# Optimization experiments

Measured on AMD Instinct MI355X. Metric: run time of the kernel, lower is better.

Reference implementation:

```python
import jax, jax.numpy as jnp
import numpy as np

N_ENT = 100000   # n_entities
N_REL = 40       # n_relations_ckg
D = 64           # embed_dim
L = 3            # n_layers
E = 1000000      # number of CKG triples (edges)


def setup_inputs() -> dict:
    key = jax.random.key(0)
    k = jax.random.split(key, 6)
    xavier = np.sqrt(6.0 / (D + D))  # xavier_uniform for square Linear
    return {
        "heads": jax.random.randint(k[0], (E,), 0, N_ENT),
        "rels": jax.random.randint(k[1], (E,), 0, N_REL),
        "tails": jax.random.randint(k[2], (E,), 0, N_ENT),
        "entity_embed": 0.01 * jax.random.normal(k[3], (N_ENT, D), dtype=jnp.float32),
        "rel_embeds": 0.01 * jax.random.normal(k[4], (L, N_REL, D), dtype=jnp.float32),
        "Ws": (jax.random.uniform(k[5], (L, D, D), minval=-1.0, maxval=1.0) * xavier).astype(jnp.float32),
    }


def _kgat_layer(h, heads, rels, tails, rel_emb, W):
    # h: [N, D]; heads/rels/tails: [E]; rel_emb: [n_rel, D]; W: [D, D] (nn.Linear weight)
    n = h.shape[0]
    e_h = h[heads]            # [E, D] gather
    e_t = h[tails]            # [E, D] gather
    e_r = rel_emb[rels]       # [E, D] gather
    # pi(h,r,t) = e_t . tanh(e_h + e_r)
    score = jnp.sum(e_t * jnp.tanh(e_h + e_r), axis=-1)          # [E]
    score = score - jax.lax.stop_gradient(jnp.max(score))        # global shift (detach)
    score_exp = jnp.exp(score)                                   # [E]
    score_sum = jax.ops.segment_sum(score_exp, heads, num_segments=n)  # [N]
    attn = score_exp / (score_sum[heads] + 1e-10)                # [E] per-head softmax
    agg = jax.ops.segment_sum(attn[:, None] * e_t, heads, num_segments=n)  # [N, D]
    out = (h + agg) @ W.T                                        # Linear, no bias
    return jax.nn.leaky_relu(out, negative_slope=0.2)            # dropout = identity (eval)


def reference(heads, rels, tails, entity_embed, rel_embeds, Ws):
    h = entity_embed
    all_layers = [h]
    for l in range(rel_embeds.shape[0]):
        h = _kgat_layer(h, heads, rels, tails, rel_embeds[l], Ws[l])
        all_layers.append(h)
    return jnp.concatenate(all_layers, axis=-1)  # [N, D*(L+1)]
```

## Files before the change

kernel.cpp:

```cpp
#include <hip/hip_runtime.h>

#define DD 64
#define ROW 256
#define CAP 32
#define CAPSH 5

__global__ void k_build(const float* __restrict__ ent, float* __restrict__ out,
                        const int* __restrict__ heads, const int* __restrict__ rels,
                        const int* __restrict__ tails, int* __restrict__ counts,
                        int* __restrict__ ovf, int* __restrict__ permpos,
                        int* __restrict__ packedF, int n_rows, int nE) {
    int idx = blockIdx.x * blockDim.x + threadIdx.x;
    int total = n_rows * 16;
    if (idx < total) {
        int n = idx >> 4, q = idx & 15;
        const float4* src = (const float4*)(ent + (long)n * DD);
        float4* dst = (float4*)(out + (long)n * ROW);
        dst[q] = src[q];
    }
    if (idx < nE) {
        int h = heads[idx];
        int rank = atomicAdd(counts + h, 1);
        permpos[idx] = rank;
        if (rank < CAP) packedF[((long)h << CAPSH) + rank] = tails[idx] | (rels[idx] << 20);
        else *ovf = 1;
    }
}

__global__ __launch_bounds__(1024) void k_fallback(
        const int* __restrict__ heads, const int* __restrict__ rels,
        const int* __restrict__ tails, const int* __restrict__ counts,
        const int* __restrict__ ovf, int* __restrict__ offs,
        const int* __restrict__ permpos, int* __restrict__ packed,
        int n, int nE) {
    if (*ovf == 0) return;
    __shared__ int lds[1024];
    int t = threadIdx.x;
    int per = (n + 1023) / 1024;
    int lo = t * per, hi = min(lo + per, n);
    int sum = 0;
    for (int i = lo; i < hi; ++i) sum += counts[i];
    lds[t] = sum; __syncthreads();
    for (int d = 1; d < 1024; d <<= 1) {
        int u = (t >= d) ? lds[t - d] : 0;
        __syncthreads();
        lds[t] += u;
        __syncthreads();
    }
    int run = lds[t] - sum;
    for (int i = lo; i < hi; ++i) { offs[i] = run; run += counts[i]; }
    if (t == 0) offs[n] = nE;
    __syncthreads();
    for (int e = t; e < nE; e += 1024) {
        int h = heads[e];
        packed[offs[h] + permpos[e]] = tails[e] | (rels[e] << 20);
    }
}

__global__ __launch_bounds__(256) void k_layer(
        const int* __restrict__ offs, const int* __restrict__ counts,
        const int* __restrict__ ovf, const int* __restrict__ packed,
        const float* __restrict__ hbase, const float* __restrict__ relemb,
        const float* __restrict__ W, float* __restrict__ outbase,
        int n_heads, int nE) {
    __shared__ float Wt[DD * 65];
    __shared__ float xs[4][DD];
    const int mode = *ovf;
    for (int idx = threadIdx.x; idx < DD * DD; idx += 256)
        Wt[(idx & 63) * 65 + (idx >> 6)] = W[idx];
    __syncthreads();

    const int cap = (n_heads << CAPSH) - 1;

    int w = threadIdx.x >> 6, lane = threadIdx.x & 63;
    int g = lane >> 4, s = lane & 15;

    for (int hd = blockIdx.x * 4 + w; hd < n_heads; hd += gridDim.x * 4) {
        int p0 = (mode == 0) ? (hd << CAPSH) : offs[hd];
        int vAll = packed[min(p0 + lane, cap)];
        int pe = (mode == 0) ? p0 + counts[hd] : offs[hd + 1];
        const float4 eh4 = *(const float4*)(hbase + (long)hd * ROW + 4 * s);
        float4 acc = make_float4(0.f, 0.f, 0.f, 0.f);
        float ssum = 0.f;

        for (int cbase = p0; cbase < pe; cbase += 64) {
            int clen = min(pe - cbase, 64);

            int i0 = (g < clen) ? g : 0;
            int i1 = (4 + g < clen) ? 4 + g : 0;
            int v0 = __shfl(vAll, i0);
            int v1 = __shfl(vAll, i1);
            float4 tt0 = *(const float4*)(hbase + (long)(v0 & 0xFFFFF) * ROW + 4 * s);
            float4 rr0 = *(const float4*)(relemb + (v0 >> 20) * DD + 4 * s);
            float4 tt1 = *(const float4*)(hbase + (long)(v1 & 0xFFFFF) * ROW + 4 * s);
            float4 rr1 = *(const float4*)(relemb + (v1 >> 20) * DD + 4 * s);

            for (int i = 0; i < clen; i += 8) {
                int ia = i + 8 + g;  ia = (ia < clen) ? ia : 0;
                int ib = i + 12 + g; ib = (ib < clen) ? ib : 0;
                int va = __shfl(vAll, ia);
                int vb = __shfl(vAll, ib);
                float4 tta = *(const float4*)(hbase + (long)(va & 0xFFFFF) * ROW + 4 * s);
                float4 rra = *(const float4*)(relemb + (va >> 20) * DD + 4 * s);
                float4 ttb = *(const float4*)(hbase + (long)(vb & 0xFFFFF) * ROW + 4 * s);
                float4 rrb = *(const float4*)(relemb + (vb >> 20) * DD + 4 * s);

                {
                    float sc = 0.f;
                    #pragma unroll
                    for (int q = 0; q < 4; ++q) {
                        float xq = (&eh4.x)[q] + (&rr0.x)[q];
                        float t = __expf(2.f * xq);
                        float th = 1.f - 2.f * __builtin_amdgcn_rcpf(t + 1.f);
                        sc += (&tt0.x)[q] * th;
                    }
                    #pragma unroll
                    for (int off = 1; off <= 8; off <<= 1) sc += __shfl_xor(sc, off);
                    float se = ((i + g) < clen) ? __expf(sc) : 0.f;
                    ssum += se;
                    acc.x += se * tt0.x; acc.y += se * tt0.y;
                    acc.z += se * tt0.z; acc.w += se * tt0.w;
                }
                {
                    float sc = 0.f;
                    #pragma unroll
                    for (int q = 0; q < 4; ++q) {
                        float xq = (&eh4.x)[q] + (&rr1.x)[q];
                        float t = __expf(2.f * xq);
                        float th = 1.f - 2.f * __builtin_amdgcn_rcpf(t + 1.f);
                        sc += (&tt1.x)[q] * th;
                    }
                    #pragma unroll
                    for (int off = 1; off <= 8; off <<= 1) sc += __shfl_xor(sc, off);
                    float se = ((i + 4 + g) < clen) ? __expf(sc) : 0.f;
                    ssum += se;
                    acc.x += se * tt1.x; acc.y += se * tt1.y;
                    acc.z += se * tt1.z; acc.w += se * tt1.w;
                }
                tt0 = tta; rr0 = rra; tt1 = ttb; rr1 = rrb;
            }

            if (cbase + 64 < pe) vAll = packed[min(cbase + 64 + lane, cap)];
        }

        #pragma unroll
        for (int off = 16; off <= 32; off <<= 1) {
            acc.x += __shfl_xor(acc.x, off);
            acc.y += __shfl_xor(acc.y, off);
            acc.z += __shfl_xor(acc.z, off);
            acc.w += __shfl_xor(acc.w, off);
            ssum  += __shfl_xor(ssum,  off);
        }
        float inv = 1.f / (ssum + 1e-10f);
        float4 x4;
        x4.x = eh4.x + acc.x * inv;  x4.y = eh4.y + acc.y * inv;
        x4.z = eh4.z + acc.z * inv;  x4.w = eh4.w + acc.w * inv;
        if (g == 0) *(float4*)(&xs[w][4 * s]) = x4;

        float y = 0.f;
        const float* xw = xs[w];
        #pragma unroll
        for (int k4 = 0; k4 < DD; k4 += 4) {
            float4 xv = *(const float4*)(xw + k4);
            y += xv.x * Wt[(k4 + 0) * 65 + lane];
            y += xv.y * Wt[(k4 + 1) * 65 + lane];
            y += xv.z * Wt[(k4 + 2) * 65 + lane];
            y += xv.w * Wt[(k4 + 3) * 65 + lane];
        }
        y = y >= 0.f ? y : 0.2f * y;
        outbase[(long)hd * ROW + lane] = y;
    }
}

extern "C" void kernel_launch(void* const* d_in, const int* in_sizes, int n_in,
                              void* d_out, int out_size, void* d_ws, size_t ws_size,
                              hipStream_t stream) {
    const int*   heads = (const int*)d_in[0];
    const int*   rels  = (const int*)d_in[1];
    const int*   tails = (const int*)d_in[2];
    const float* ent   = (const float*)d_in[3];
    const float* rel   = (const float*)d_in[4];
    const float* Ws    = (const float*)d_in[5];
    float* out = (float*)d_out;

    const int nE = in_sizes[0];
    const int N  = in_sizes[3] / DD;
    const int L  = in_sizes[5] / (DD * DD);
    const int NREL = in_sizes[4] / (L * DD);

    int* counts  = (int*)d_ws;
    int* ovf     = counts + N;
    int* offs    = ovf + 1;
    int* permpos = offs + (N + 1);
    int* packedF = permpos + nE;

    dim3 blk(256);
    int fuse_total = max(N * 16, nE);

    hipMemsetAsync(counts, 0, (size_t)(N + 1) * sizeof(int), stream);
    k_build<<<(fuse_total + 255) / 256, blk, 0, stream>>>(
        ent, out, heads, rels, tails, counts, ovf, permpos, packedF, N, nE);
    k_fallback<<<1, 1024, 0, stream>>>(
        heads, rels, tails, counts, ovf, offs, permpos, packedF, N, nE);

    for (int l = 0; l < L; ++l) {
        k_layer<<<2048, blk, 0, stream>>>(
            offs, counts, ovf, packedF, out + l * DD, rel + (long)l * NREL * DD,
            Ws + (long)l * DD * DD, out + (l + 1) * DD, N, nE);
    }
}
```

Before: 445.2 us.

## Use odd polynomial tanh when inputs are small, fuse entity copy into first layer

Computes the per-layer max |rel_emb| and, per head, the max |e_h|. When their sum stays below a bound, tanh is evaluated with an odd polynomial instead of exp plus reciprocal, with a plain loop kept as the fallback. The first layer now reads the entity table directly with a 64-float stride and writes the layer-0 slice of the output itself, so the separate copy pass disappears. The permpos array is dropped and the overflow path uses atomic cursors instead. The polynomial's accuracy depends on the range bound, which holds for small-magnitude embeddings like the test data.

```diff
diff --git a/kernel.cpp b/kernel.cpp
--- a/kernel.cpp
+++ b/kernel.cpp
@@ -4,35 +4,38 @@
 #define ROW 256
 #define CAP 32
 #define CAPSH 5
-
-__global__ void k_build(const float* __restrict__ ent, float* __restrict__ out,
-                        const int* __restrict__ heads, const int* __restrict__ rels,
+#define POLY_R 0.625f
+
+__global__ __launch_bounds__(256) void k_relmax(const float* __restrict__ rel,
+                                                float* __restrict__ maxrel, int per) {
+    __shared__ float red[256];
+    int t = threadIdx.x, l = blockIdx.x;
+    float m = 0.f;
+    for (int i = t; i < per; i += 256) m = fmaxf(m, __builtin_fabsf(rel[(long)l * per + i]));
+    red[t] = m; __syncthreads();
+    for (int d = 128; d > 0; d >>= 1) {
+        if (t < d) red[t] = fmaxf(red[t], red[t + d]);
+        __syncthreads();
+    }
+    if (t == 0) maxrel[l] = red[0];
+}
+
+__global__ void k_build(const int* __restrict__ heads, const int* __restrict__ rels,
                         const int* __restrict__ tails, int* __restrict__ counts,
-                        int* __restrict__ ovf, int* __restrict__ permpos,
-                        int* __restrict__ packedF, int n_rows, int nE) {
-    int idx = blockIdx.x * blockDim.x + threadIdx.x;
-    int total = n_rows * 16;
-    if (idx < total) {
-        int n = idx >> 4, q = idx & 15;
-        const float4* src = (const float4*)(ent + (long)n * DD);
-        float4* dst = (float4*)(out + (long)n * ROW);
-        dst[q] = src[q];
-    }
-    if (idx < nE) {
-        int h = heads[idx];
-        int rank = atomicAdd(counts + h, 1);
-        permpos[idx] = rank;
-        if (rank < CAP) packedF[((long)h << CAPSH) + rank] = tails[idx] | (rels[idx] << 20);
-        else *ovf = 1;
-    }
+                        int* __restrict__ ovf, int* __restrict__ packedF, int nE) {
+    int e = blockIdx.x * 256 + threadIdx.x;
+    if (e >= nE) return;
+    int h = heads[e];
+    int rank = atomicAdd(counts + h, 1);
+    if (rank < CAP) packedF[((long)h << CAPSH) + rank] = tails[e] | (rels[e] << 20);
+    else *ovf = 1;
 }
 
 __global__ __launch_bounds__(1024) void k_fallback(
         const int* __restrict__ heads, const int* __restrict__ rels,
         const int* __restrict__ tails, const int* __restrict__ counts,
         const int* __restrict__ ovf, int* __restrict__ offs,
-        const int* __restrict__ permpos, int* __restrict__ packed,
-        int n, int nE) {
+        int* __restrict__ cursors, int* __restrict__ packed, int n, int nE) {
     if (*ovf == 0) return;
     __shared__ int lds[1024];
     int t = threadIdx.x;
@@ -48,28 +51,34 @@
         __syncthreads();
     }
     int run = lds[t] - sum;
-    for (int i = lo; i < hi; ++i) { offs[i] = run; run += counts[i]; }
+    for (int i = lo; i < hi; ++i) { offs[i] = run; cursors[i] = run; run += counts[i]; }
     if (t == 0) offs[n] = nE;
     __syncthreads();
     for (int e = t; e < nE; e += 1024) {
-        int h = heads[e];
-        packed[offs[h] + permpos[e]] = tails[e] | (rels[e] << 20);
+        int pos = atomicAdd(cursors + heads[e], 1);
+        packed[pos] = tails[e] | (rels[e] << 20);
     }
 }
 
 __global__ __launch_bounds__(256) void k_layer(
         const int* __restrict__ offs, const int* __restrict__ counts,
         const int* __restrict__ ovf, const int* __restrict__ packed,
-        const float* __restrict__ hbase, const float* __restrict__ relemb,
+        const float* __restrict__ src, int srcsh, float* __restrict__ copy0,
+        const float* __restrict__ maxrel, const float* __restrict__ relemb,
         const float* __restrict__ W, float* __restrict__ outbase,
-        int n_heads, int nE) {
+        int n_heads) {
     __shared__ float Wt[DD * 65];
     __shared__ float xs[4][DD];
     const int mode = *ovf;
+    const float mr = *maxrel;
     for (int idx = threadIdx.x; idx < DD * DD; idx += 256)
         Wt[(idx & 63) * 65 + (idx >> 6)] = W[idx];
     __syncthreads();
 
+    const float c11 = -5.70498872745e-3f, c9 = 2.06390887954e-2f,
+                c7  = -5.37397155531e-2f, c5 = 1.33314422036e-1f,
+                c3  = -3.33332819422e-1f;
+
     const int cap = (n_heads << CAPSH) - 1;
 
     int w = threadIdx.x >> 6, lane = threadIdx.x & 63;
@@ -77,70 +86,117 @@
 
     for (int hd = blockIdx.x * 4 + w; hd < n_heads; hd += gridDim.x * 4) {
         int p0 = (mode == 0) ? (hd << CAPSH) : offs[hd];
-        int vAll = packed[min(p0 + lane, cap)];
+        int li = (mode == 0) ? (lane & 31) : lane;
+        int vAll = packed[min(p0 + li, cap)];
         int pe = (mode == 0) ? p0 + counts[hd] : offs[hd + 1];
-        const float4 eh4 = *(const float4*)(hbase + (long)hd * ROW + 4 * s);
+        const float4 eh4 = *(const float4*)(src + ((long)hd << srcsh) + 4 * s);
         float4 acc = make_float4(0.f, 0.f, 0.f, 0.f);
         float ssum = 0.f;
 
-        for (int cbase = p0; cbase < pe; cbase += 64) {
-            int clen = min(pe - cbase, 64);
-
-            int i0 = (g < clen) ? g : 0;
-            int i1 = (4 + g < clen) ? 4 + g : 0;
-            int v0 = __shfl(vAll, i0);
-            int v1 = __shfl(vAll, i1);
-            float4 tt0 = *(const float4*)(hbase + (long)(v0 & 0xFFFFF) * ROW + 4 * s);
-            float4 rr0 = *(const float4*)(relemb + (v0 >> 20) * DD + 4 * s);
-            float4 tt1 = *(const float4*)(hbase + (long)(v1 & 0xFFFFF) * ROW + 4 * s);
-            float4 rr1 = *(const float4*)(relemb + (v1 >> 20) * DD + 4 * s);
-
-            for (int i = 0; i < clen; i += 8) {
-                int ia = i + 8 + g;  ia = (ia < clen) ? ia : 0;
-                int ib = i + 12 + g; ib = (ib < clen) ? ib : 0;
-                int va = __shfl(vAll, ia);
-                int vb = __shfl(vAll, ib);
-                float4 tta = *(const float4*)(hbase + (long)(va & 0xFFFFF) * ROW + 4 * s);
-                float4 rra = *(const float4*)(relemb + (va >> 20) * DD + 4 * s);
-                float4 ttb = *(const float4*)(hbase + (long)(vb & 0xFFFFF) * ROW + 4 * s);
-                float4 rrb = *(const float4*)(relemb + (vb >> 20) * DD + 4 * s);
-
-                {
-                    float sc = 0.f;
-                    #pragma unroll
-                    for (int q = 0; q < 4; ++q) {
-                        float xq = (&eh4.x)[q] + (&rr0.x)[q];
-                        float t = __expf(2.f * xq);
-                        float th = 1.f - 2.f * __builtin_amdgcn_rcpf(t + 1.f);
-                        sc += (&tt0.x)[q] * th;
+        float axh = fmaxf(fmaxf(__builtin_fabsf(eh4.x), __builtin_fabsf(eh4.y)),
+                          fmaxf(__builtin_fabsf(eh4.z), __builtin_fabsf(eh4.w)));
+        #pragma unroll
+        for (int off = 1; off <= 8; off <<= 1) axh = fmaxf(axh, __shfl_xor(axh, off));
+
+        if (axh + mr > POLY_R) {
+            for (int p = p0 + g; p < pe; p += 4) {
+                int v = packed[p];
+                float4 tt = *(const float4*)(src + ((long)(v & 0xFFFFF) << srcsh) + 4 * s);
+                float4 rr = *(const float4*)(relemb + (v >> 20) * DD + 4 * s);
+                float sc = 0.f;
+                #pragma unroll
+                for (int q = 0; q < 4; ++q) {
+                    float x = (&eh4.x)[q] + (&rr.x)[q];
+                    float t = __expf(2.f * x);
+                    float th = 1.f - 2.f * __builtin_amdgcn_rcpf(t + 1.f);
+                    sc = fmaf((&tt.x)[q], th, sc);
+                }
+                #pragma unroll
+                for (int off = 1; off <= 8; off <<= 1) sc += __shfl_xor(sc, off);
+                float se = __expf(sc);
+                ssum += se;
+                acc.x = fmaf(se, tt.x, acc.x);
+                acc.y = fmaf(se, tt.y, acc.y);
+                acc.z = fmaf(se, tt.z, acc.z);
+                acc.w = fmaf(se, tt.w, acc.w);
+            }
+        } else {
+            for (int cbase = p0; cbase < pe; cbase += 64) {
+                int clen = min(pe - cbase, 64);
+
+                int i0 = (g < clen) ? g : 0;
+                int i1 = (4 + g < clen) ? 4 + g : 0;
+                int v0 = __shfl(vAll, i0);
+                int v1 = __shfl(vAll, i1);
+                float4 tt0 = *(const float4*)(src + ((long)(v0 & 0xFFFFF) << srcsh) + 4 * s);
+                float4 rr0 = *(const float4*)(relemb + (v0 >> 20) * DD + 4 * s);
+                float4 tt1 = *(const float4*)(src + ((long)(v1 & 0xFFFFF) << srcsh) + 4 * s);
+                float4 rr1 = *(const float4*)(relemb + (v1 >> 20) * DD + 4 * s);
+
+                for (int i = 0; i < clen; i += 8) {
+                    float4 tta, rra, ttb, rrb;
+                    if (i + 8 < clen) {
+                        int ia = i + 8 + g;  ia = (ia < clen) ? ia : 0;
+                        int ib = i + 12 + g; ib = (ib < clen) ? ib : 0;
+                        int va = __shfl(vAll, ia);
+                        int vb = __shfl(vAll, ib);
+                        tta = *(const float4*)(src + ((long)(va & 0xFFFFF) << srcsh) + 4 * s);
+                        rra = *(const float4*)(relemb + (va >> 20) * DD + 4 * s);
+                        ttb = *(const float4*)(src + ((long)(vb & 0xFFFFF) << srcsh) + 4 * s);
+                        rrb = *(const float4*)(relemb + (vb >> 20) * DD + 4 * s);
+                    } else {
+                        tta = tt0; rra = rr0; ttb = tt1; rrb = rr1;
                     }
-                    #pragma unroll
-                    for (int off = 1; off <= 8; off <<= 1) sc += __shfl_xor(sc, off);
-                    float se = ((i + g) < clen) ? __expf(sc) : 0.f;
-                    ssum += se;
-                    acc.x += se * tt0.x; acc.y += se * tt0.y;
-                    acc.z += se * tt0.z; acc.w += se * tt0.w;
+
+                    {
+                        float sc = 0.f;
+                        #pragma unroll
+                        for (int q = 0; q < 4; ++q) {
+                            float x = (&eh4.x)[q] + (&rr0.x)[q];
+                            float z = x * x;
+                            float p = fmaf(z, c11, c9);
+                            p = fmaf(z, p, c7);
+                            p = fmaf(z, p, c5);
+                            p = fmaf(z, p, c3);
+                            float th = fmaf(x * z, p, x);
+                            sc = fmaf((&tt0.x)[q], th, sc);
+                        }
+                        #pragma unroll
+                        for (int off = 1; off <= 8; off <<= 1) sc += __shfl_xor(sc, off);
+                        float se = ((i + g) < clen) ? __expf(sc) : 0.f;
+                        ssum += se;
+                        acc.x = fmaf(se, tt0.x, acc.x);
+                        acc.y = fmaf(se, tt0.y, acc.y);
+                        acc.z = fmaf(se, tt0.z, acc.z);
+                        acc.w = fmaf(se, tt0.w, acc.w);
+                    }
+                    {
+                        float sc = 0.f;
+                        #pragma unroll
+                        for (int q = 0; q < 4; ++q) {
+                            float x = (&eh4.x)[q] + (&rr1.x)[q];
+                            float z = x * x;
+                            float p = fmaf(z, c11, c9);
+                            p = fmaf(z, p, c7);
+                            p = fmaf(z, p, c5);
+                            p = fmaf(z, p, c3);
+                            float th = fmaf(x * z, p, x);
+                            sc = fmaf((&tt1.x)[q], th, sc);
+                        }
+                        #pragma unroll
+                        for (int off = 1; off <= 8; off <<= 1) sc += __shfl_xor(sc, off);
+                        float se = ((i + 4 + g) < clen) ? __expf(sc) : 0.f;
+                        ssum += se;
+                        acc.x = fmaf(se, tt1.x, acc.x);
+                        acc.y = fmaf(se, tt1.y, acc.y);
+                        acc.z = fmaf(se, tt1.z, acc.z);
+                        acc.w = fmaf(se, tt1.w, acc.w);
+                    }
+                    tt0 = tta; rr0 = rra; tt1 = ttb; rr1 = rrb;
                 }
-                {
-                    float sc = 0.f;
-                    #pragma unroll
-                    for (int q = 0; q < 4; ++q) {
-                        float xq = (&eh4.x)[q] + (&rr1.x)[q];
-                        float t = __expf(2.f * xq);
-                        float th = 1.f - 2.f * __builtin_amdgcn_rcpf(t + 1.f);
-                        sc += (&tt1.x)[q] * th;
-                    }
-                    #pragma unroll
-                    for (int off = 1; off <= 8; off <<= 1) sc += __shfl_xor(sc, off);
-                    float se = ((i + 4 + g) < clen) ? __expf(sc) : 0.f;
-                    ssum += se;
-                    acc.x += se * tt1.x; acc.y += se * tt1.y;
-                    acc.z += se * tt1.z; acc.w += se * tt1.w;
-                }
-                tt0 = tta; rr0 = rra; tt1 = ttb; rr1 = rrb;
+
+                if (cbase + 64 < pe) vAll = packed[min(cbase + 64 + lane, cap)];
             }
-
-            if (cbase + 64 < pe) vAll = packed[min(cbase + 64 + lane, cap)];
         }
 
         #pragma unroll
@@ -169,6 +225,8 @@
         }
         y = y >= 0.f ? y : 0.2f * y;
         outbase[(long)hd * ROW + lane] = y;
+        if (copy0 != nullptr && g == 0)
+            *(float4*)(copy0 + (long)hd * ROW + 4 * s) = eh4;
     }
 }
 
@@ -188,24 +246,29 @@
     const int L  = in_sizes[5] / (DD * DD);
     const int NREL = in_sizes[4] / (L * DD);
 
-    int* counts  = (int*)d_ws;
-    int* ovf     = counts + N;
-    int* offs    = ovf + 1;
-    int* permpos = offs + (N + 1);
-    int* packedF = permpos + nE;
+    int*   counts  = (int*)d_ws;
+    int*   ovf     = counts + N;
+    float* maxrel  = (float*)(ovf + 1);
+    int*   offs    = (int*)(maxrel + 4);
+    int*   cursors = offs + (N + 1);
+    int*   packedF = cursors + N;
 
     dim3 blk(256);
-    int fuse_total = max(N * 16, nE);
 
     hipMemsetAsync(counts, 0, (size_t)(N + 1) * sizeof(int), stream);
-    k_build<<<(fuse_total + 255) / 256, blk, 0, stream>>>(
-        ent, out, heads, rels, tails, counts, ovf, permpos, packedF, N, nE);
+    k_relmax<<<L, blk, 0, stream>>>(rel, maxrel, NREL * DD);
+    k_build<<<(nE + 255) / 256, blk, 0, stream>>>(
+        heads, rels, tails, counts, ovf, packedF, nE);
     k_fallback<<<1, 1024, 0, stream>>>(
-        heads, rels, tails, counts, ovf, offs, permpos, packedF, N, nE);
+        heads, rels, tails, counts, ovf, offs, cursors, packedF, N, nE);
 
     for (int l = 0; l < L; ++l) {
+        const float* src = (l == 0) ? ent : (out + l * DD);
+        int srcsh = (l == 0) ? 6 : 8;
+        float* copy0 = (l == 0) ? out : (float*)nullptr;
         k_layer<<<2048, blk, 0, stream>>>(
-            offs, counts, ovf, packedF, out + l * DD, rel + (long)l * NREL * DD,
-            Ws + (long)l * DD * DD, out + (l + 1) * DD, N, nE);
-    }
-}
+            offs, counts, ovf, packedF, src, srcsh, copy0, maxrel + l,
+            rel + (long)l * NREL * DD, Ws + (long)l * DD * DD,
+            out + (l + 1) * DD, N);
+    }
+}
```

After: 546.4 us. 22.7% more time.
